# Kernel tuning notes

Measured on AMD Instinct MI355X. Metric: run time of the kernel, lower is better.

The kernel has to match this reference:

```python
import jax, jax.numpy as jnp
import numpy as np

MAX_NUM_POINTS = 2048
MAX_NUM_PERSONS = 8
CHUNK = 1024  # matches torch chunk_size


def setup_inputs() -> dict:
    key = jax.random.key(0)
    k1, k2 = jax.random.split(key)
    shape = (4, 3, (MAX_NUM_POINTS + 1) * MAX_NUM_PERSONS)
    return {
        "predictions": jax.random.normal(k1, shape, dtype=jnp.float32),
        "targets": jax.random.normal(k2, shape, dtype=jnp.float32),
    }


def _one_direction(a, b):
    # a, b: [B, N, 3]; for each point in a, min euclidean distance to b, summed over N.
    B, N, _ = a.shape
    b_sq = jnp.sum(b * b, axis=-1)  # [B, N]
    chunks = a.reshape(B, N // CHUNK, CHUNK, 3).transpose(1, 0, 2, 3)  # [n_chunks, B, C, 3]

    def step(carry, chunk):  # chunk: [B, C, 3]
        a_sq = jnp.sum(chunk * chunk, axis=-1)  # [B, C]
        d2 = a_sq[:, :, None] + b_sq[:, None, :] - 2.0 * jnp.einsum('bcd,bnd->bcn', chunk, b)
        d = jnp.sqrt(jnp.maximum(d2, 0.0))  # [B, C, N]
        return carry + jnp.sum(jnp.min(d, axis=2), axis=1), None

    total, _ = jax.lax.scan(step, jnp.zeros((B,), a.dtype), chunks)
    return total / N  # [B]


def _chamfer(pred, tgt):
    # pred, tgt: [B, N, 3]
    return jnp.mean((_one_direction(pred, tgt) + _one_direction(tgt, pred)) * 0.5)


def reference(predictions, targets):
    B = predictions.shape[0]
    P, K = MAX_NUM_POINTS, MAX_NUM_PERSONS
    x = predictions.reshape(B, 3, K, P + 1)
    y = targets.reshape(B, 3, K, P + 1)

    pred_indicator = x[:, 0, :, P]  # [B, K] logits
    target_indicator = (y[:, 0, :, P] > 0.5).astype(jnp.float32)  # [B, K]

    # BCEWithLogitsLoss, mean reduction (numerically stable form)
    z, t = pred_indicator, target_indicator
    detection_loss = jnp.mean(jnp.maximum(z, 0.0) - z * t + jnp.log1p(jnp.exp(-jnp.abs(z))))

    # clouds: [B, 3, K, P] -> [B, K*P, 3] (point order irrelevant for chamfer)
    pred_cloud = x[:, :, :, :P].transpose(0, 2, 3, 1).reshape(B, K * P, 3)
    target_cloud = y[:, :, :, :P].transpose(0, 2, 3, 1).reshape(B, K * P, 3)

    point_cloud_loss = _chamfer(pred_cloud, target_cloud)
    return detection_loss + point_cloud_loss
```

## Files before the change

### kernel.cpp

```cpp
#include <hip/hip_runtime.h>
#include <math.h>

#define PP 2048
#define KK 8
#define BB 4
#define NN 16384
#define CSTRIDE 16392
#define BSTRIDE 49176

#define FRAGS 8
#define ROWS_PER_BLOCK 1024
#define ROWBLOCKS 16
#define NSLICES 8
#define SLICEPTS 2048
#define CHUNKPTS 1024
#define TILES 32

typedef _Float16 f16;
typedef __attribute__((ext_vector_type(8))) _Float16 f16x8;
typedef __attribute__((ext_vector_type(16))) float f32x16;

__device__ __forceinline__ float min3f(float a, float b, float c) {
    return fminf(fminf(a, b), c);
}

__device__ __forceinline__ void fold16(const f32x16& d, float& a) {
    float m0 = min3f(d[0],  d[1],  d[2]);
    float m1 = min3f(d[3],  d[4],  d[5]);
    float m2 = min3f(d[6],  d[7],  d[8]);
    float m3 = min3f(d[9],  d[10], d[11]);
    float m4 = min3f(d[12], d[13], d[14]);
    float n0 = min3f(m0, m1, m2);
    float n1 = min3f(m3, m4, d[15]);
    a = min3f(a, n0, n1);
}

__global__ __launch_bounds__(256) void init_min_kernel(unsigned* __restrict__ mins) {
    int i = blockIdx.x * 256 + threadIdx.x;
    mins[i] = 0x7F7FFFFFu;
}

__global__ __launch_bounds__(256, 2) void chamfer_mfma_kernel(
        const float* __restrict__ pred, const float* __restrict__ tgt,
        unsigned* __restrict__ mins) {
    __shared__ f16x8 karr[2 * CHUNKPTS];

    const int tid  = threadIdx.x;
    const int lane = tid & 63;
    const int wave = tid >> 6;
    const int col  = lane & 31;
    const int g2   = lane >> 5;
    const int dir  = blockIdx.z >> 2;
    const int b    = blockIdx.z & 3;
    const int slice = blockIdx.y;
    const int rowblock = blockIdx.x;

    const float* __restrict__ Apts = dir ? tgt : pred;
    const float* __restrict__ Bpts = dir ? pred : tgt;
    unsigned* __restrict__ minOut = mins + dir * BB * NN;

    f16x8 bop[FRAGS];
    float asq[FRAGS], acc[FRAGS];
    const int rbase = rowblock * ROWS_PER_BLOCK + wave * (FRAGS * 32);
#pragma unroll
    for (int f = 0; f < FRAGS; ++f) {
        int r = rbase + f * 32 + col;
        int abase = b * BSTRIDE + (r >> 11) * (PP + 1) + (r & (PP - 1));
        float ax = Apts[abase];
        float ay = Apts[abase + CSTRIDE];
        float az = Apts[abase + 2 * CSTRIDE];
        asq[f] = fmaf(ax, ax, fmaf(ay, ay, az * az));
        acc[f] = 1.0e30f;
        f16 h0 = (f16)ax, h1 = (f16)ay, h2 = (f16)az;
        f16 l0 = (f16)(ax - (float)h0);
        f16 l1 = (f16)(ay - (float)h1);
        f16 l2 = (f16)(az - (float)h2);
        f16x8 v;
#pragma unroll
        for (int j = 0; j < 8; ++j) v[j] = (f16)0.f;
        if (g2 == 0) {
            v[0] = -h0; v[1] = -h1; v[2] = -h2;
            v[3] = -h0; v[4] = -h1; v[5] = -h2;
            v[6] = -l0; v[7] = -l1;
        } else {
            v[0] = -l2; v[1] = (f16)1.f; v[2] = (f16)1.f;
        }
        bop[f] = v;
    }

    f32x16 Z16;
#pragma unroll
    for (int j = 0; j < 16; ++j) Z16[j] = 0.f;

    for (int c = 0; c < SLICEPTS / CHUNKPTS; ++c) {
        __syncthreads();
#pragma unroll
        for (int q = 0; q < 4; ++q) {
            int p  = tid + q * 256;
            int cj = slice * SLICEPTS + c * CHUNKPTS + p;
            int gb = b * BSTRIDE + (cj >> 11) * (PP + 1) + (cj & (PP - 1));
            float x = Bpts[gb];
            float y = Bpts[gb + CSTRIDE];
            float z = Bpts[gb + 2 * CSTRIDE];
            f16 h0 = (f16)x, h1 = (f16)y, h2 = (f16)z;
            f16 l0 = (f16)(x - (float)h0);
            f16 l1 = (f16)(y - (float)h1);
            f16 l2 = (f16)(z - (float)h2);
            float bsq = 0.5f * fmaf(x, x, fmaf(y, y, z * z));
            f16 sh = (f16)bsq;
            f16 sl = (f16)(bsq - (float)sh);
            f16x8 lo;
            lo[0] = h0; lo[1] = h1; lo[2] = h2;
            lo[3] = l0; lo[4] = l1; lo[5] = l2;
            lo[6] = h0; lo[7] = h1;
            f16x8 hi;
#pragma unroll
            for (int j = 0; j < 8; ++j) hi[j] = (f16)0.f;
            hi[0] = h2; hi[1] = sh; hi[2] = sl;
            karr[p] = lo;
            karr[CHUNKPTS + p] = hi;
        }
        __syncthreads();

        const f16x8* kptr = karr + g2 * CHUNKPTS + col;
#pragma unroll 2
        for (int t = 0; t < TILES; ++t) {
            f16x8 af = kptr[t * 32];
            f32x16 d0, d1, d2;
            d0 = __builtin_amdgcn_mfma_f32_32x32x16_f16(af, bop[0], Z16, 0, 0, 0);
            d1 = __builtin_amdgcn_mfma_f32_32x32x16_f16(af, bop[1], Z16, 0, 0, 0);
            d2 = __builtin_amdgcn_mfma_f32_32x32x16_f16(af, bop[2], Z16, 0, 0, 0);
            fold16(d0, acc[0]);
            d0 = __builtin_amdgcn_mfma_f32_32x32x16_f16(af, bop[3], Z16, 0, 0, 0);
            fold16(d1, acc[1]);
            d1 = __builtin_amdgcn_mfma_f32_32x32x16_f16(af, bop[4], Z16, 0, 0, 0);
            fold16(d2, acc[2]);
            d2 = __builtin_amdgcn_mfma_f32_32x32x16_f16(af, bop[5], Z16, 0, 0, 0);
            fold16(d0, acc[3]);
            d0 = __builtin_amdgcn_mfma_f32_32x32x16_f16(af, bop[6], Z16, 0, 0, 0);
            fold16(d1, acc[4]);
            d1 = __builtin_amdgcn_mfma_f32_32x32x16_f16(af, bop[7], Z16, 0, 0, 0);
            fold16(d2, acc[5]);
            fold16(d0, acc[6]);
            fold16(d1, acc[7]);
        }
    }

#pragma unroll
    for (int f = 0; f < FRAGS; ++f) {
        float m = acc[f];
        m = fminf(m, __shfl_xor(m, 32));
        if (lane < 32) {
            float d2v = fmaxf(fmaf(2.0f, m, asq[f]), 0.0f);
            atomicMin(&minOut[b * NN + rbase + f * 32 + col], __float_as_uint(d2v));
        }
    }
}

__global__ __launch_bounds__(1024) void reduce_final_kernel(
        const unsigned* __restrict__ mins,
        const float* __restrict__ pred, const float* __restrict__ tgt,
        float* __restrict__ out) {
    int tid = threadIdx.x;
    const uint4* m4 = (const uint4*)mins;
    float s = 0.f;
    for (int i = tid; i < (2 * BB * NN) / 4; i += 1024) {
        uint4 u = m4[i];
        s += sqrtf(__uint_as_float(u.x)) + sqrtf(__uint_as_float(u.y)) +
             sqrtf(__uint_as_float(u.z)) + sqrtf(__uint_as_float(u.w));
    }
    float v = s * (1.0f / 131072.0f);
    if (tid < 32) {
        int b = tid >> 3, k = tid & 7;
        int idx = b * BSTRIDE + k * (PP + 1) + PP;
        float z = pred[idx];
        float t = tgt[idx] > 0.5f ? 1.0f : 0.0f;
        v += (fmaxf(z, 0.f) - z * t + log1pf(expf(-fabsf(z)))) * (1.0f / 32.0f);
    }
    __shared__ float red[1024];
    red[tid] = v;
    __syncthreads();
    for (int off = 512; off > 0; off >>= 1) {
        if (tid < off) red[tid] += red[tid + off];
        __syncthreads();
    }
    if (tid == 0) out[0] = red[0];
}

extern "C" void kernel_launch(void* const* d_in, const int* in_sizes, int n_in,
                              void* d_out, int out_size, void* d_ws, size_t ws_size,
                              hipStream_t stream) {
    const float* pred = (const float*)d_in[0];
    const float* tgt  = (const float*)d_in[1];
    float* out = (float*)d_out;

    unsigned* mins = (unsigned*)d_ws;

    init_min_kernel<<<2 * BB * NN / 256, 256, 0, stream>>>(mins);
    dim3 grid(ROWBLOCKS, NSLICES, 2 * BB);
    chamfer_mfma_kernel<<<grid, 256, 0, stream>>>(pred, tgt, mins);
    reduce_final_kernel<<<1, 1024, 0, stream>>>(mins, pred, tgt, out);
}
```

Measured before the change: 85.12 us.

## Use inline-asm MFMA with zero accumulator and parallelize final reduction

Replaces the MFMA builtin calls, which took an explicit zero accumulator register set, with inline assembly that uses a literal 0 for C. This frees the 16 VGPRs that held Z16 and removes their initialisation. The single-block 1024-thread final reduction becomes 64 blocks that add fixed-point partial sums with 64-bit atomics, and the last block to arrive (by ticket counter) computes the output. The fixed-point accumulation keeps the result deterministic, but the volatile asm may limit how the compiler schedules the MFMAs.

```diff
diff --git a/kernel.cpp b/kernel.cpp
--- a/kernel.cpp
+++ b/kernel.cpp
@@ -15,10 +15,18 @@
 #define SLICEPTS 2048
 #define CHUNKPTS 1024
 #define TILES 32
+#define RBLK 64
 
 typedef _Float16 f16;
 typedef __attribute__((ext_vector_type(8))) _Float16 f16x8;
 typedef __attribute__((ext_vector_type(16))) float f32x16;
+
+__device__ __forceinline__ f32x16 mfma_z(f16x8 a, f16x8 b) {
+    f32x16 d;
+    asm volatile("v_mfma_f32_32x32x16_f16 %0, %1, %2, 0"
+                 : "=v"(d) : "v"(a), "v"(b));
+    return d;
+}
 
 __device__ __forceinline__ float min3f(float a, float b, float c) {
     return fminf(fminf(a, b), c);
@@ -35,9 +43,12 @@
     a = min3f(a, n0, n1);
 }
 
-__global__ __launch_bounds__(256) void init_min_kernel(unsigned* __restrict__ mins) {
+__global__ __launch_bounds__(256) void init_min_kernel(
+        unsigned* __restrict__ mins, unsigned long long* __restrict__ sum,
+        unsigned* __restrict__ ticket) {
     int i = blockIdx.x * 256 + threadIdx.x;
     mins[i] = 0x7F7FFFFFu;
+    if (i == 0) { *sum = 0ULL; *ticket = 0u; }
 }
 
 __global__ __launch_bounds__(256, 2) void chamfer_mfma_kernel(
@@ -87,10 +98,6 @@
         }
         bop[f] = v;
     }
-
-    f32x16 Z16;
-#pragma unroll
-    for (int j = 0; j < 16; ++j) Z16[j] = 0.f;
 
     for (int c = 0; c < SLICEPTS / CHUNKPTS; ++c) {
         __syncthreads();
@@ -127,19 +134,19 @@
         for (int t = 0; t < TILES; ++t) {
             f16x8 af = kptr[t * 32];
             f32x16 d0, d1, d2;
-            d0 = __builtin_amdgcn_mfma_f32_32x32x16_f16(af, bop[0], Z16, 0, 0, 0);
-            d1 = __builtin_amdgcn_mfma_f32_32x32x16_f16(af, bop[1], Z16, 0, 0, 0);
-            d2 = __builtin_amdgcn_mfma_f32_32x32x16_f16(af, bop[2], Z16, 0, 0, 0);
+            d0 = mfma_z(af, bop[0]);
+            d1 = mfma_z(af, bop[1]);
+            d2 = mfma_z(af, bop[2]);
             fold16(d0, acc[0]);
-            d0 = __builtin_amdgcn_mfma_f32_32x32x16_f16(af, bop[3], Z16, 0, 0, 0);
+            d0 = mfma_z(af, bop[3]);
             fold16(d1, acc[1]);
-            d1 = __builtin_amdgcn_mfma_f32_32x32x16_f16(af, bop[4], Z16, 0, 0, 0);
+            d1 = mfma_z(af, bop[4]);
             fold16(d2, acc[2]);
-            d2 = __builtin_amdgcn_mfma_f32_32x32x16_f16(af, bop[5], Z16, 0, 0, 0);
+            d2 = mfma_z(af, bop[5]);
             fold16(d0, acc[3]);
-            d0 = __builtin_amdgcn_mfma_f32_32x32x16_f16(af, bop[6], Z16, 0, 0, 0);
+            d0 = mfma_z(af, bop[6]);
             fold16(d1, acc[4]);
-            d1 = __builtin_amdgcn_mfma_f32_32x32x16_f16(af, bop[7], Z16, 0, 0, 0);
+            d1 = mfma_z(af, bop[7]);
             fold16(d2, acc[5]);
             fold16(d0, acc[6]);
             fold16(d1, acc[7]);
@@ -157,34 +164,45 @@
     }
 }
 
-__global__ __launch_bounds__(1024) void reduce_final_kernel(
-        const unsigned* __restrict__ mins,
+__global__ __launch_bounds__(256) void reduce_kernel(
+        const unsigned* __restrict__ mins, unsigned long long* __restrict__ sum,
+        unsigned* __restrict__ ticket,
         const float* __restrict__ pred, const float* __restrict__ tgt,
         float* __restrict__ out) {
     int tid = threadIdx.x;
     const uint4* m4 = (const uint4*)mins;
     float s = 0.f;
-    for (int i = tid; i < (2 * BB * NN) / 4; i += 1024) {
+    for (int i = blockIdx.x * 256 + tid; i < (2 * BB * NN) / 4; i += RBLK * 256) {
         uint4 u = m4[i];
         s += sqrtf(__uint_as_float(u.x)) + sqrtf(__uint_as_float(u.y)) +
              sqrtf(__uint_as_float(u.z)) + sqrtf(__uint_as_float(u.w));
     }
-    float v = s * (1.0f / 131072.0f);
-    if (tid < 32) {
-        int b = tid >> 3, k = tid & 7;
-        int idx = b * BSTRIDE + k * (PP + 1) + PP;
-        float z = pred[idx];
-        float t = tgt[idx] > 0.5f ? 1.0f : 0.0f;
-        v += (fmaxf(z, 0.f) - z * t + log1pf(expf(-fabsf(z)))) * (1.0f / 32.0f);
-    }
-    __shared__ float red[1024];
-    red[tid] = v;
+    __shared__ float red[256];
+    red[tid] = s;
     __syncthreads();
-    for (int off = 512; off > 0; off >>= 1) {
+    for (int off = 128; off > 0; off >>= 1) {
         if (tid < off) red[tid] += red[tid + off];
         __syncthreads();
     }
-    if (tid == 0) out[0] = red[0];
+    if (tid == 0) {
+        unsigned long long fx = (unsigned long long)((double)red[0] * 1099511627776.0);
+        atomicAdd(sum, fx);
+        __threadfence();
+        unsigned prev = atomicAdd(ticket, 1u);
+        if (prev == RBLK - 1) {
+            unsigned long long tot = atomicAdd(sum, 0ULL);
+            float v = (float)((double)tot * (1.0 / 1099511627776.0) * (1.0 / 131072.0));
+            float det = 0.f;
+            for (int j = 0; j < 32; ++j) {
+                int bb = j >> 3, k = j & 7;
+                int idx = bb * BSTRIDE + k * (PP + 1) + PP;
+                float z = pred[idx];
+                float t = tgt[idx] > 0.5f ? 1.0f : 0.0f;
+                det += fmaxf(z, 0.f) - z * t + log1pf(expf(-fabsf(z)));
+            }
+            out[0] = v + det * (1.0f / 32.0f);
+        }
+    }
 }
 
 extern "C" void kernel_launch(void* const* d_in, const int* in_sizes, int n_in,
@@ -195,9 +213,11 @@
     float* out = (float*)d_out;
 
     unsigned* mins = (unsigned*)d_ws;
-
-    init_min_kernel<<<2 * BB * NN / 256, 256, 0, stream>>>(mins);
+    unsigned long long* sum = (unsigned long long*)((char*)d_ws + 2 * BB * NN * 4);
+    unsigned* ticket = (unsigned*)((char*)d_ws + 2 * BB * NN * 4 + 8);
+
+    init_min_kernel<<<2 * BB * NN / 256, 256, 0, stream>>>(mins, sum, ticket);
     dim3 grid(ROWBLOCKS, NSLICES, 2 * BB);
     chamfer_mfma_kernel<<<grid, 256, 0, stream>>>(pred, tgt, mins);
-    reduce_final_kernel<<<1, 1024, 0, stream>>>(mins, pred, tgt, out);
-}
+    reduce_kernel<<<RBLK, 256, 0, stream>>>(mins, sum, ticket, pred, tgt, out);
+}
```

Measured after the change: 83.53 us. Within noise of the previous version (-1.9%).
